# Performance work log

Measured on AMD Instinct MI355X. Metric: run time of the kernel, lower is better.

## Reference

```python
import jax, jax.numpy as jnp
import numpy as np

B, C, O, K, H, W, CH = 32, 256, 256, 3, 56, 56, 4  # batch, in_planes, out_planes, kernel, spatial, in_chunk
STRIDE, PAD, DIL = 1, 1, 1


def setup_inputs() -> dict:
    key = jax.random.key(0)
    ks = jax.random.split(key, 5)
    gain = np.sqrt(2.0).astype(np.float32)  # calculate_gain('relu')
    x = jax.random.normal(ks[0], (B, C, H, W), jnp.float32)
    # CWFF: fc1 1x1 conv (C->C, no bias), fc2 1x1 conv (C->CH*C, bias)
    fc1_w = jax.random.normal(ks[1], (C, C), jnp.float32) * np.sqrt(2.0 / C).astype(np.float32)  # kaiming fan_out
    fc2_w = jax.random.normal(ks[2], (CH * C, C), jnp.float32) * np.sqrt(2.0 / (CH * C)).astype(np.float32)
    fc2_b = jnp.zeros((CH * C,), jnp.float32)
    cog_weight = jax.random.normal(ks[3], (O, CH, K, K), jnp.float32) * (gain * (CH * K * K) ** -0.5)
    weight = jax.random.normal(ks[4], (O, C, K, K), jnp.float32) * (gain * (C * K * K) ** -0.5)
    return dict(x=x, fc1_w=fc1_w, fc2_w=fc2_w, fc2_b=fc2_b, cog_weight=cog_weight, weight=weight)


def reference(x, fc1_w, fc2_w, fc2_b, cog_weight, weight):
    # CWFF: global avg pool -> 1x1 conv -> relu -> 1x1 conv
    pooled = x.mean(axis=(2, 3))                       # [B, C]
    h = jax.nn.relu(pooled @ fc1_w.T)                  # [B, C]
    kern = h @ fc2_w.T + fc2_b                         # [B, CH*C]
    # torch view(-1, in_chunk, 1, 1): channel dim splits as (c, ch)
    kern = kern.reshape(B, C, CH)                      # [B, C, CH]
    # cognitive weights: conv2d(cog_weight, kernel) == contraction over in_chunk
    cw = jnp.einsum('bct,otij->bocij', kern, cog_weight)   # [B, O, C, K, K]
    dyn_w = jax.nn.sigmoid(cw) * weight[None]               # per-sample kernels [B, O, C, K, K]
    # per-sample conv (groups=B in the original grouped-conv trick)
    def conv1(xi, wi):
        return jax.lax.conv_general_dilated(
            xi[None], wi,
            window_strides=(STRIDE, STRIDE),
            padding=[(PAD, PAD), (PAD, PAD)],
            rhs_dilation=(DIL, DIL))[0]
    return jax.vmap(conv1)(x, dyn_w)                   # [B, O, H, W]
```

## Files before the change

kernel.cpp:

```cpp
#include <hip/hip_runtime.h>

typedef unsigned short u16;
typedef __attribute__((ext_vector_type(4))) float f32x4;
typedef __attribute__((ext_vector_type(8))) short s16x8;
typedef __attribute__((ext_vector_type(4))) unsigned short u16x4;

static __device__ __forceinline__ u16 f2bf(float f) {
    unsigned int x = __float_as_uint(f);
    x += 0x7fffu + ((x >> 16) & 1u);
    return (u16)(x >> 16);
}

__global__ __launch_bounds__(256) void pool_kernel(const float* __restrict__ x,
                                                   float* __restrict__ pooled) {
    int bc = blockIdx.x;
    const float* p = x + (size_t)bc * 3136;
    float s = 0.f;
    for (int i = threadIdx.x; i < 784; i += 256) {
        f32x4 v = *(const f32x4*)(p + i * 4);
        s += v.x + v.y + v.z + v.w;
    }
#pragma unroll
    for (int off = 32; off; off >>= 1) s += __shfl_xor(s, off);
    __shared__ float red[4];
    int lane = threadIdx.x & 63, wave = threadIdx.x >> 6;
    if (lane == 0) red[wave] = s;
    __syncthreads();
    if (threadIdx.x == 0)
        pooled[bc] = (red[0] + red[1] + red[2] + red[3]) * (1.0f / 3136.0f);
}

__global__ __launch_bounds__(256) void fc1_kernel(const float* __restrict__ pooled,
                                                  const float* __restrict__ w,
                                                  float* __restrict__ h) {
    __shared__ float pv[256];
    int b = blockIdx.x >> 6;
    pv[threadIdx.x] = pooled[b * 256 + threadIdx.x];
    __syncthreads();
    int lane = threadIdx.x & 63, wave = threadIdx.x >> 6;
    int i = ((blockIdx.x & 63) << 2) + wave;
    f32x4 v = *(const f32x4*)(w + i * 256 + lane * 4);
    float s = v.x * pv[lane * 4 + 0] + v.y * pv[lane * 4 + 1] +
              v.z * pv[lane * 4 + 2] + v.w * pv[lane * 4 + 3];
#pragma unroll
    for (int off = 32; off; off >>= 1) s += __shfl_xor(s, off);
    if (lane == 0) h[b * 256 + i] = fmaxf(s, 0.f);
}

__global__ __launch_bounds__(256) void fc2_kernel(const float* __restrict__ h,
                                                  const float* __restrict__ w,
                                                  const float* __restrict__ bias,
                                                  float* __restrict__ kern) {
    __shared__ float hv[256];
    int b = blockIdx.x >> 8;
    hv[threadIdx.x] = h[b * 256 + threadIdx.x];
    __syncthreads();
    int lane = threadIdx.x & 63, wave = threadIdx.x >> 6;
    int i = ((blockIdx.x & 255) << 2) + wave;
    f32x4 v = *(const f32x4*)(w + i * 256 + lane * 4);
    float s = v.x * hv[lane * 4 + 0] + v.y * hv[lane * 4 + 1] +
              v.z * hv[lane * 4 + 2] + v.w * hv[lane * 4 + 3];
#pragma unroll
    for (int off = 32; off; off >>= 1) s += __shfl_xor(s, off);
    if (lane == 0) kern[b * 1024 + i] = s + bias[i];
}

__global__ __launch_bounds__(256) void dynw_kernel(const float* __restrict__ kern,
                                                   const float* __restrict__ cogw,
                                                   const float* __restrict__ wgt,
                                                   u16* __restrict__ dynw) {
    __shared__ float wl[2304];
    const int o = blockIdx.x & 255;
    const int bg = blockIdx.x >> 8;
    const int c = threadIdx.x;
    const float* wo = wgt + (size_t)o * 2304;
#pragma unroll
    for (int j = 0; j < 9; ++j)
        wl[j * 256 + c] = wo[j * 256 + c];
    __syncthreads();

    float cg0[9], cg1[9], cg2[9], cg3[9];
#pragma unroll
    for (int p = 0; p < 9; ++p) {
        cg0[p] = cogw[(o * 4 + 0) * 9 + p];
        cg1[p] = cogw[(o * 4 + 1) * 9 + p];
        cg2[p] = cogw[(o * 4 + 2) * 9 + p];
        cg3[p] = cogw[(o * 4 + 3) * 9 + p];
    }
    float w9[9];
#pragma unroll
    for (int p = 0; p < 9; ++p) w9[p] = wl[c * 9 + p];

    for (int b = bg * 8; b < bg * 8 + 8; ++b) {
        f32x4 k4 = *(const f32x4*)(kern + b * 1024 + c * 4);
        u16* dst = dynw + (size_t)(b * 256 + o) * 9 * 256 + c;
#pragma unroll
        for (int p = 0; p < 9; ++p) {
            float cw = k4.x * cg0[p] + k4.y * cg1[p] + k4.z * cg2[p] + k4.w * cg3[p];
            float sg = 1.0f / (1.0f + __expf(-cw));
            dst[p * 256] = f2bf(sg * w9[p]);
        }
    }
}

#define LDSW 40
__global__ __launch_bounds__(256, 2) void conv_kernel(const float* __restrict__ x,
                                                      const u16* __restrict__ dynw,
                                                      float* __restrict__ out) {
    __shared__ u16 lds[4 * 58 * LDSW];
    const int tid = threadIdx.x;
    const int wave = tid >> 6, lane = tid & 63;
    const int l15 = lane & 15, quad = lane >> 4;
    const int gid = blockIdx.x;
    const int slot = gid >> 3;
    const int b = (gid & 7) * 4 + slot / 28;
    const int stile = slot % 28;
    const int y0 = stile * 2;

    if (tid < 64) {
        int side = tid & 1, yy = (tid >> 1) & 3, cg = tid >> 3;
        *(u16x4*)&lds[(yy * 58 + (side ? 57 : 0)) * LDSW + cg * 4] = (u16x4){0, 0, 0, 0};
    }

    f32x4 acc[4][7];
#pragma unroll
    for (int mf = 0; mf < 4; ++mf)
#pragma unroll
        for (int nf = 0; nf < 7; ++nf) acc[mf][nf] = (f32x4){0.f, 0.f, 0.f, 0.f};

    int bbase[7];
#pragma unroll
    for (int nf = 0; nf < 7; ++nf) {
        int n = nf * 16 + l15;
        int r = (n >= 56) ? 1 : 0;
        int xx = n - 56 * r;
        bbase[nf] = (r * 58 + xx) * LDSW + quad * 8;
    }
    const u16* Abase = dynw + ((size_t)b * 256 + wave * 64 + l15) * 2304 + quad * 8;
    const float* Xb = x + (size_t)b * 256 * 3136;

    __syncthreads();
    for (int cc = 0; cc < 8; ++cc) {
#pragma unroll
        for (int it = 0; it < 7; ++it) {
            int i = it * 256 + tid;
            int q = i / 56;
            int xx = i - q * 56;
            int yy = q & 3;
            int cg = q >> 2;
            int yg = y0 - 1 + yy;
            u16x4 w = (u16x4){0, 0, 0, 0};
            if ((unsigned)yg < 56u) {
                const float* src = Xb + (size_t)(cc * 32 + cg * 4) * 3136 + yg * 56 + xx;
                w.x = f2bf(src[0]);
                w.y = f2bf(src[3136]);
                w.z = f2bf(src[2 * 3136]);
                w.w = f2bf(src[3 * 3136]);
            }
            *(u16x4*)&lds[(yy * 58 + 1 + xx) * LDSW + cg * 4] = w;
        }
        __syncthreads();
#pragma unroll
        for (int p = 0; p < 9; ++p) {
            const int dy = p / 3, dx = p % 3;
            const int tapoff = (dy * 58 + dx) * LDSW;
            s16x8 a0 = *(const s16x8*)(Abase + 0 * 36864 + p * 256 + cc * 32);
            s16x8 a1 = *(const s16x8*)(Abase + 1 * 36864 + p * 256 + cc * 32);
            s16x8 a2 = *(const s16x8*)(Abase + 2 * 36864 + p * 256 + cc * 32);
            s16x8 a3 = *(const s16x8*)(Abase + 3 * 36864 + p * 256 + cc * 32);
#pragma unroll
            for (int nf = 0; nf < 7; ++nf) {
                s16x8 bf = *(const s16x8*)(&lds[bbase[nf] + tapoff]);
                acc[0][nf] = __builtin_amdgcn_mfma_f32_16x16x32_bf16(a0, bf, acc[0][nf], 0, 0, 0);
                acc[1][nf] = __builtin_amdgcn_mfma_f32_16x16x32_bf16(a1, bf, acc[1][nf], 0, 0, 0);
                acc[2][nf] = __builtin_amdgcn_mfma_f32_16x16x32_bf16(a2, bf, acc[2][nf], 0, 0, 0);
                acc[3][nf] = __builtin_amdgcn_mfma_f32_16x16x32_bf16(a3, bf, acc[3][nf], 0, 0, 0);
            }
        }
        __syncthreads();
    }
#pragma unroll
    for (int mf = 0; mf < 4; ++mf) {
        int o = wave * 64 + mf * 16 + quad * 4;
        size_t obase = ((size_t)b * 256 + o) * 3136 + (size_t)stile * 112 + l15;
#pragma unroll
        for (int nf = 0; nf < 7; ++nf) {
#pragma unroll
            for (int r = 0; r < 4; ++r)
                out[obase + (size_t)r * 3136 + nf * 16] = acc[mf][nf][r];
        }
    }
}

extern "C" void kernel_launch(void* const* d_in, const int* in_sizes, int n_in,
                              void* d_out, int out_size, void* d_ws, size_t ws_size,
                              hipStream_t stream) {
    const float* x    = (const float*)d_in[0];
    const float* fc1w = (const float*)d_in[1];
    const float* fc2w = (const float*)d_in[2];
    const float* fc2b = (const float*)d_in[3];
    const float* cogw = (const float*)d_in[4];
    const float* wgt  = (const float*)d_in[5];
    float* out = (float*)d_out;

    char* ws = (char*)d_ws;
    float* pooled = (float*)ws;
    float* h      = (float*)(ws + 32768);
    float* kern   = (float*)(ws + 65536);
    u16*   dynw   = (u16*)(ws + 196608);

    pool_kernel<<<8192, 256, 0, stream>>>(x, pooled);
    fc1_kernel<<<2048, 256, 0, stream>>>(pooled, fc1w, h);
    fc2_kernel<<<8192, 256, 0, stream>>>(h, fc2w, fc2b, kern);
    dynw_kernel<<<1024, 256, 0, stream>>>(kern, cogw, wgt, dynw);
    conv_kernel<<<896, 256, 0, stream>>>(x, dynw, out);
}
```

Baseline: 384.6 us.

## Double-buffer conv input tile in LDS and swizzle channel groups

Turns the conv kernel's single LDS input tile into two buffers. Global loads for the next channel chunk are issued during the MFMA loop of the current chunk and written to LDS two taps later, which removes one barrier per chunk and overlaps load latency with compute. It also XOR-swizzles the channel-group position within each LDS row to cut bank conflicts on the B-fragment reads. The cost is double the LDS footprint (about 18.5 KB per block), which may limit occupancy, plus more registers for the staged values.

```diff
diff --git a/kernel.cpp b/kernel.cpp
--- a/kernel.cpp
+++ b/kernel.cpp
@@ -107,7 +107,7 @@
 __global__ __launch_bounds__(256, 2) void conv_kernel(const float* __restrict__ x,
                                                       const u16* __restrict__ dynw,
                                                       float* __restrict__ out) {
-    __shared__ u16 lds[4 * 58 * LDSW];
+    __shared__ u16 lds[2][4 * 58 * LDSW];
     const int tid = threadIdx.x;
     const int wave = tid >> 6, lane = tid & 63;
     const int l15 = lane & 15, quad = lane >> 4;
@@ -117,9 +117,12 @@
     const int stile = slot % 28;
     const int y0 = stile * 2;
 
-    if (tid < 64) {
-        int side = tid & 1, yy = (tid >> 1) & 3, cg = tid >> 3;
-        *(u16x4*)&lds[(yy * 58 + (side ? 57 : 0)) * LDSW + cg * 4] = (u16x4){0, 0, 0, 0};
+    if (tid < 128) {
+        int bufi = tid >> 6;
+        int t = tid & 63;
+        int side = t & 1, yy = (t >> 1) & 3, cg = t >> 3;
+        *(u16x4*)&lds[bufi][(yy * 58 + (side ? 57 : 0)) * LDSW + cg * 4] =
+            (u16x4){0, 0, 0, 0};
     }
 
     f32x4 acc[4][7];
@@ -128,57 +131,103 @@
 #pragma unroll
         for (int nf = 0; nf < 7; ++nf) acc[mf][nf] = (f32x4){0.f, 0.f, 0.f, 0.f};
 
-    int bbase[7];
+    int rowb[7], sw[7];
 #pragma unroll
     for (int nf = 0; nf < 7; ++nf) {
         int n = nf * 16 + l15;
         int r = (n >= 56) ? 1 : 0;
         int xx = n - 56 * r;
-        bbase[nf] = (r * 58 + xx) * LDSW + quad * 8;
+        rowb[nf] = (r * 58 + xx) * LDSW;
+        int s0 = (quad ^ ((xx >> 3) & 3)) << 3;
+        int s1 = (quad ^ (((xx + 1) >> 3) & 3)) << 3;
+        int s2 = (quad ^ (((xx + 2) >> 3) & 3)) << 3;
+        sw[nf] = s0 | (s1 << 6) | (s2 << 12);
     }
     const u16* Abase = dynw + ((size_t)b * 256 + wave * 64 + l15) * 2304 + quad * 8;
     const float* Xb = x + (size_t)b * 256 * 3136;
 
-    __syncthreads();
+#pragma unroll
+    for (int it = 0; it < 7; ++it) {
+        int i = it * 256 + tid;
+        int q = i / 56;
+        int xxw = i - q * 56;
+        int yy = q & 3;
+        int cg = q >> 2;
+        int col = xxw + 1;
+        int cgx = cg ^ (((col >> 3) & 3) << 1);
+        int yg = y0 - 1 + yy;
+        u16x4 w = (u16x4){0, 0, 0, 0};
+        if ((unsigned)yg < 56u) {
+            const float* src = Xb + (size_t)(cg * 4) * 3136 + yg * 56 + xxw;
+            w.x = f2bf(src[0]);
+            w.y = f2bf(src[3136]);
+            w.z = f2bf(src[2 * 3136]);
+            w.w = f2bf(src[3 * 3136]);
+        }
+        *(u16x4*)&lds[0][(yy * 58 + col) * LDSW + cgx * 4] = w;
+    }
+    __syncthreads();
+
     for (int cc = 0; cc < 8; ++cc) {
-#pragma unroll
-        for (int it = 0; it < 7; ++it) {
-            int i = it * 256 + tid;
-            int q = i / 56;
-            int xx = i - q * 56;
-            int yy = q & 3;
-            int cg = q >> 2;
-            int yg = y0 - 1 + yy;
-            u16x4 w = (u16x4){0, 0, 0, 0};
-            if ((unsigned)yg < 56u) {
-                const float* src = Xb + (size_t)(cc * 32 + cg * 4) * 3136 + yg * 56 + xx;
-                w.x = f2bf(src[0]);
-                w.y = f2bf(src[3136]);
-                w.z = f2bf(src[2 * 3136]);
-                w.w = f2bf(src[3 * 3136]);
-            }
-            *(u16x4*)&lds[(yy * 58 + 1 + xx) * LDSW + cg * 4] = w;
-        }
-        __syncthreads();
+        const u16* Lr = lds[cc & 1];
+        u16* Lw = lds[(cc & 1) ^ 1];
+        const bool more = (cc < 7);
+        float sv[3][4];
+        int soff[3];
 #pragma unroll
         for (int p = 0; p < 9; ++p) {
             const int dy = p / 3, dx = p % 3;
-            const int tapoff = (dy * 58 + dx) * LDSW;
             s16x8 a0 = *(const s16x8*)(Abase + 0 * 36864 + p * 256 + cc * 32);
             s16x8 a1 = *(const s16x8*)(Abase + 1 * 36864 + p * 256 + cc * 32);
             s16x8 a2 = *(const s16x8*)(Abase + 2 * 36864 + p * 256 + cc * 32);
             s16x8 a3 = *(const s16x8*)(Abase + 3 * 36864 + p * 256 + cc * 32);
+
+            if (more && p < 7) {
+                int i = p * 256 + tid;
+                int q = i / 56;
+                int xxw = i - q * 56;
+                int yy = q & 3;
+                int cg = q >> 2;
+                int col = xxw + 1;
+                int cgx = cg ^ (((col >> 3) & 3) << 1);
+                soff[p % 3] = (yy * 58 + col) * LDSW + cgx * 4;
+                int yg = y0 - 1 + yy;
+                float f0 = 0.f, f1 = 0.f, f2 = 0.f, f3 = 0.f;
+                if ((unsigned)yg < 56u) {
+                    const float* src =
+                        Xb + (size_t)((cc + 1) * 32 + cg * 4) * 3136 + yg * 56 + xxw;
+                    f0 = src[0];
+                    f1 = src[3136];
+                    f2 = src[2 * 3136];
+                    f3 = src[3 * 3136];
+                }
+                sv[p % 3][0] = f0; sv[p % 3][1] = f1;
+                sv[p % 3][2] = f2; sv[p % 3][3] = f3;
+            }
+
 #pragma unroll
             for (int nf = 0; nf < 7; ++nf) {
-                s16x8 bf = *(const s16x8*)(&lds[bbase[nf] + tapoff]);
+                int off = rowb[nf] + (dy * 58 + dx) * LDSW + ((sw[nf] >> (6 * dx)) & 63);
+                s16x8 bf = *(const s16x8*)(Lr + off);
                 acc[0][nf] = __builtin_amdgcn_mfma_f32_16x16x32_bf16(a0, bf, acc[0][nf], 0, 0, 0);
                 acc[1][nf] = __builtin_amdgcn_mfma_f32_16x16x32_bf16(a1, bf, acc[1][nf], 0, 0, 0);
                 acc[2][nf] = __builtin_amdgcn_mfma_f32_16x16x32_bf16(a2, bf, acc[2][nf], 0, 0, 0);
                 acc[3][nf] = __builtin_amdgcn_mfma_f32_16x16x32_bf16(a3, bf, acc[3][nf], 0, 0, 0);
             }
+
+            if (more && p >= 2) {
+                const int it = p - 2;
+                u16x4 wv;
+                wv.x = f2bf(sv[it % 3][0]);
+                wv.y = f2bf(sv[it % 3][1]);
+                wv.z = f2bf(sv[it % 3][2]);
+                wv.w = f2bf(sv[it % 3][3]);
+                *(u16x4*)(Lw + soff[it % 3]) = wv;
+            }
         }
         __syncthreads();
     }
+
 #pragma unroll
     for (int mf = 0; mf < 4; ++mf) {
         int o = wave * 64 + mf * 16 + quad * 4;
```

New measurement: 398.6 us. 1.04x slower.
